# Performance work log

Hardware: AMD Instinct MI355X
Metric: run time of the kernel (lower is better)

Reference implementation:

```python
import jax, jax.numpy as jnp
import numpy as np

BLOCK_M, BLOCK_K = 16, 64
THRES = 0.8


def setup_inputs() -> dict:
    key = jax.random.key(0)
    kx, kw = jax.random.split(key)
    bsz, seq, in_f, out_f = 128, 1, 4096, 11008
    x = jax.random.normal(kx, (bsz, seq, in_f), dtype=jnp.float16)
    # kaiming_uniform_(a=sqrt(5)) on a (in,out) weight -> bound = 1/sqrt(fan_in)
    bound = 1.0 / np.sqrt(in_f)
    weight = jax.random.uniform(kw, (in_f, out_f), dtype=jnp.float16,
                                minval=-bound, maxval=bound)
    bias = jnp.zeros((out_f,), dtype=jnp.float16)
    return {"x": x, "weight": weight, "bias": bias}


def reference(x, weight, bias):
    bsz, seq, hidden = x.shape
    x2 = x.reshape(bsz * seq, hidden)          # (M, K), seq == 1 decode path
    M, K = x2.shape
    # avg_magnitude_threshold: per (BLOCK_M, BLOCK_K) block mean |x| vs thres
    blocks = x2.reshape(M // BLOCK_M, BLOCK_M, K // BLOCK_K, BLOCK_K)
    avg = jnp.mean(jnp.abs(blocks).astype(jnp.float32), axis=(1, 3))  # (M/bm, K/bk)
    mask = avg > THRES                           # block active if avg magnitude above thres
    # blocksparse_masked_gemm: skipped blocks contribute nothing -> zero them out
    xm = jnp.where(mask[:, None, :, None], blocks, jnp.float16(0)).reshape(M, K)
    y = xm @ weight                              # (M, out_features)
    return y.reshape(bsz, seq, -1) + bias
```

## Files before the change

### kernel.cpp

```cpp
#include <hip/hip_runtime.h>
#include <stdint.h>

using f32x4   = __attribute__((ext_vector_type(4))) float;
using short8  = __attribute__((ext_vector_type(8))) short;
using float4v = __attribute__((ext_vector_type(4))) float;
using float2v = __attribute__((ext_vector_type(2))) float;
using uint2v  = __attribute__((ext_vector_type(2))) unsigned int;
using uint4v  = __attribute__((ext_vector_type(4))) unsigned int;

#define NCOL 11008
#define KDIM 4096
#define LSTRIDE 264

__device__ __forceinline__ unsigned pk_bf16(float a, float b) {
  unsigned ua = __float_as_uint(a); ua += 0x7fffu + ((ua >> 16) & 1u);
  unsigned ub = __float_as_uint(b); ub += 0x7fffu + ((ub >> 16) & 1u);
  return (ua >> 16) | (ub & 0xffff0000u);
}

__global__ __launch_bounds__(256) void mask_convert_kernel(
    const float* __restrict__ x, unsigned* __restrict__ xbf) {
  const int rb = blockIdx.x;
  const int g  = blockIdx.y;
  const int t  = threadIdx.x;
  __shared__ double part[256];
  __shared__ unsigned sh_bits;

  const float* base = x + (size_t)rb * 16 * KDIM + g * 512 + t * 2;
  double s = 0.0;
#pragma unroll
  for (int r = 0; r < 16; ++r) {
    float2v a = *(const float2v*)(base + (size_t)r * KDIM);
    s += (double)fabsf(a[0]) + (double)fabsf(a[1]);
  }
  part[t] = s;
  __syncthreads();
  if (t < 8) {
    double acc = 0.0;
#pragma unroll
    for (int u = 0; u < 32; ++u) acc += part[t * 32 + u];
    bool on = (acc * (1.0 / 1024.0)) > (double)0.8f;
    unsigned long long bal = __ballot(on);
    if (t == 0) sh_bits = (unsigned)(bal & 0xffu);
  }
  __syncthreads();
  const unsigned keep = (sh_bits >> (t >> 5)) & 1u;

  unsigned* dst = xbf + (size_t)rb * 16 * (KDIM / 2) + g * 256 + t;
#pragma unroll
  for (int r = 0; r < 16; ++r) {
    float2v a = *(const float2v*)(base + (size_t)r * KDIM);
    dst[(size_t)r * (KDIM / 2)] = keep ? pk_bf16(a[0], a[1]) : 0u;
  }
}

__global__ __launch_bounds__(256) void gemm_kernel(
    const unsigned* __restrict__ xbf, const float* __restrict__ w,
    const float* __restrict__ bias, float* __restrict__ out) {

  __shared__ __align__(16) uint8_t lds[64 * LSTRIDE];

  const int tid  = threadIdx.x;
  const int lane = tid & 63;
  const int wv   = tid >> 6;
  const int c    = lane & 15;
  const int q    = lane >> 4;
  const int n0   = blockIdx.x * 128;
  const int kz   = blockIdx.y;

  f32x4 acc[8][2] = {};

  const int sk = tid >> 5;
  const int sn = (tid & 31) * 4;
  uint8_t* wS = lds + (size_t)sk * LSTRIDE + sn * 2;

  float4v wr[8];
#define ISSUE_W(KB)                                                      \
  {                                                                      \
    const float* wp = w + (size_t)(kz * 512 + (KB)*64 + sk) * NCOL + n0 + sn; \
    _Pragma("unroll")                                                    \
    for (int r = 0; r < 8; ++r)                                          \
      wr[r] = *(const float4v*)(wp + (size_t)r * 8 * NCOL);              \
  }

  const uint4v* aBase = (const uint4v*)xbf + (size_t)c * 512 + kz * 64 + q;

  ISSUE_W(0);
  for (int kb = 0; kb < 8; ++kb) {
    __syncthreads();
#pragma unroll
    for (int r = 0; r < 8; ++r) {
      uint2v v;
      v[0] = pk_bf16(wr[r][0], wr[r][1]);
      v[1] = pk_bf16(wr[r][2], wr[r][3]);
      *(uint2v*)(wS + (size_t)r * 8 * LSTRIDE) = v;
    }
    __syncthreads();
    if (kb < 7) ISSUE_W(kb + 1);

#pragma unroll
    for (int ks = 0; ks < 2; ++ks) {
      union { uint4v u; short8 v; } am[8];
#pragma unroll
      for (int mt = 0; mt < 8; ++mt)
        am[mt].u = aBase[(size_t)mt * 16 * 512 + kb * 8 + ks * 4];

      const uint8_t* wb = lds + (size_t)(ks * 32 + q * 8) * LSTRIDE + (wv * 32 + 2 * c) * 2;
      unsigned wj[8];
#pragma unroll
      for (int j = 0; j < 8; ++j)
        wj[j] = *(const unsigned*)(wb + (size_t)j * LSTRIDE);
      union { short8 v; unsigned u[4]; } be, bo;
#pragma unroll
      for (int p = 0; p < 4; ++p) {
        be.u[p] = (wj[2 * p] & 0x0000ffffu) | (wj[2 * p + 1] << 16);
        bo.u[p] = (wj[2 * p] >> 16) | (wj[2 * p + 1] & 0xffff0000u);
      }
#pragma unroll
      for (int mt = 0; mt < 8; ++mt) {
        acc[mt][0] = __builtin_amdgcn_mfma_f32_16x16x32_bf16(am[mt].v, be.v, acc[mt][0], 0, 0, 0);
        acc[mt][1] = __builtin_amdgcn_mfma_f32_16x16x32_bf16(am[mt].v, bo.v, acc[mt][1], 0, 0, 0);
      }
    }
  }
#undef ISSUE_W

  const int colE = n0 + wv * 32 + 2 * c;
  const float bE = (kz == 0) ? bias[colE] : 0.f;
  const float bO = (kz == 0) ? bias[colE + 1] : 0.f;
#pragma unroll
  for (int mt = 0; mt < 8; ++mt) {
#pragma unroll
    for (int p = 0; p < 4; ++p) {
      const int row = mt * 16 + q * 4 + p;
      float* o = out + (size_t)row * NCOL + colE;
      unsafeAtomicAdd(o,     acc[mt][0][p] + bE);
      unsafeAtomicAdd(o + 1, acc[mt][1][p] + bO);
    }
  }
}

extern "C" void kernel_launch(void* const* d_in, const int* in_sizes, int n_in,
                              void* d_out, int out_size, void* d_ws, size_t ws_size,
                              hipStream_t stream) {
  const float* x    = (const float*)d_in[0];
  const float* w    = (const float*)d_in[1];
  const float* bias = (const float*)d_in[2];
  float* out        = (float*)d_out;
  unsigned* xbf     = (unsigned*)d_ws;

  hipLaunchKernelGGL(mask_convert_kernel, dim3(8, 8), dim3(256), 0, stream, x, xbf);
  hipMemsetAsync(out, 0, (size_t)out_size * sizeof(float), stream);
  hipLaunchKernelGGL(gemm_kernel, dim3(86, 8), dim3(256), 0, stream,
                     xbf, w, bias, out);
}
```

Before: 329.9 us.

## Replace split-K atomics with per-row-block full-K tiles and direct stores

Changes the GEMM decomposition from split-K over 8 slices to one block per 16-row by 128-column tile running over the full K dimension. This removes the output memset and the atomic accumulation, replacing them with plain vectorized stores. In exchange, each weight tile is loaded and converted from fp32 to bf16 eight times, once per row block, instead of once. Each K step also does far fewer MFMAs between barriers, and the K loop is eight times longer.

```diff
diff --git a/kernel.cpp b/kernel.cpp
--- a/kernel.cpp
+++ b/kernel.cpp
@@ -65,28 +65,28 @@
   const int wv   = tid >> 6;
   const int c    = lane & 15;
   const int q    = lane >> 4;
-  const int n0   = blockIdx.x * 128;
-  const int kz   = blockIdx.y;
+  const int rb   = blockIdx.x;
+  const int n0   = blockIdx.y * 128;
 
-  f32x4 acc[8][2] = {};
+  f32x4 acc[2] = {};
 
   const int sk = tid >> 5;
   const int sn = (tid & 31) * 4;
   uint8_t* wS = lds + (size_t)sk * LSTRIDE + sn * 2;
 
+  const uint4v* aBase = (const uint4v*)xbf + (size_t)(rb * 16 + c) * (KDIM / 8) + q;
+
   float4v wr[8];
 #define ISSUE_W(KB)                                                      \
   {                                                                      \
-    const float* wp = w + (size_t)(kz * 512 + (KB)*64 + sk) * NCOL + n0 + sn; \
+    const float* wp = w + (size_t)((KB)*64 + sk) * NCOL + n0 + sn;       \
     _Pragma("unroll")                                                    \
     for (int r = 0; r < 8; ++r)                                          \
       wr[r] = *(const float4v*)(wp + (size_t)r * 8 * NCOL);              \
   }
 
-  const uint4v* aBase = (const uint4v*)xbf + (size_t)c * 512 + kz * 64 + q;
-
   ISSUE_W(0);
-  for (int kb = 0; kb < 8; ++kb) {
+  for (int kb = 0; kb < 64; ++kb) {
     __syncthreads();
 #pragma unroll
     for (int r = 0; r < 8; ++r) {
@@ -96,14 +96,12 @@
       *(uint2v*)(wS + (size_t)r * 8 * LSTRIDE) = v;
     }
     __syncthreads();
-    if (kb < 7) ISSUE_W(kb + 1);
+    if (kb < 63) ISSUE_W(kb + 1);
 
 #pragma unroll
     for (int ks = 0; ks < 2; ++ks) {
-      union { uint4v u; short8 v; } am[8];
-#pragma unroll
-      for (int mt = 0; mt < 8; ++mt)
-        am[mt].u = aBase[(size_t)mt * 16 * 512 + kb * 8 + ks * 4];
+      union { uint4v u; short8 v; } am;
+      am.u = aBase[kb * 8 + ks * 4];
 
       const uint8_t* wb = lds + (size_t)(ks * 32 + q * 8) * LSTRIDE + (wv * 32 + 2 * c) * 2;
       unsigned wj[8];
@@ -116,27 +114,22 @@
         be.u[p] = (wj[2 * p] & 0x0000ffffu) | (wj[2 * p + 1] << 16);
         bo.u[p] = (wj[2 * p] >> 16) | (wj[2 * p + 1] & 0xffff0000u);
       }
-#pragma unroll
-      for (int mt = 0; mt < 8; ++mt) {
-        acc[mt][0] = __builtin_amdgcn_mfma_f32_16x16x32_bf16(am[mt].v, be.v, acc[mt][0], 0, 0, 0);
-        acc[mt][1] = __builtin_amdgcn_mfma_f32_16x16x32_bf16(am[mt].v, bo.v, acc[mt][1], 0, 0, 0);
-      }
+      acc[0] = __builtin_amdgcn_mfma_f32_16x16x32_bf16(am.v, be.v, acc[0], 0, 0, 0);
+      acc[1] = __builtin_amdgcn_mfma_f32_16x16x32_bf16(am.v, bo.v, acc[1], 0, 0, 0);
     }
   }
 #undef ISSUE_W
 
   const int colE = n0 + wv * 32 + 2 * c;
-  const float bE = (kz == 0) ? bias[colE] : 0.f;
-  const float bO = (kz == 0) ? bias[colE + 1] : 0.f;
+  const float bE = bias[colE];
+  const float bO = bias[colE + 1];
 #pragma unroll
-  for (int mt = 0; mt < 8; ++mt) {
-#pragma unroll
-    for (int p = 0; p < 4; ++p) {
-      const int row = mt * 16 + q * 4 + p;
-      float* o = out + (size_t)row * NCOL + colE;
-      unsafeAtomicAdd(o,     acc[mt][0][p] + bE);
-      unsafeAtomicAdd(o + 1, acc[mt][1][p] + bO);
-    }
+  for (int p = 0; p < 4; ++p) {
+    const int row = rb * 16 + q * 4 + p;
+    float2v st;
+    st[0] = acc[0][p] + bE;
+    st[1] = acc[1][p] + bO;
+    *(float2v*)(out + (size_t)row * NCOL + colE) = st;
   }
 }
 
@@ -150,7 +143,6 @@
   unsigned* xbf     = (unsigned*)d_ws;
 
   hipLaunchKernelGGL(mask_convert_kernel, dim3(8, 8), dim3(256), 0, stream, x, xbf);
-  hipMemsetAsync(out, 0, (size_t)out_size * sizeof(float), stream);
-  hipLaunchKernelGGL(gemm_kernel, dim3(86, 8), dim3(256), 0, stream,
+  hipLaunchKernelGGL(gemm_kernel, dim3(8, 86), dim3(256), 0, stream,
                      xbf, w, bias, out);
 }
```

New measurement: 412.3 us. 1.25x slower.

## Replace split-K atomic GEMM with per-block intra-block K split and LDS reduction

Applied to the files above, without the earlier changes.

The grid changes from an 86x8 split-K launch (4 waves per block, atomic adds into a memset output) to 344 blocks of 2 waves. Each block owns 32 output columns, and its two waves split K into interleaved halves. Each wave stages bf16-converted weights in a private double-buffered LDS region with a 2-deep register prefetch and no block barriers. The partial sums are combined through LDS and written with plain stores plus bias, which removes the memset and the roughly 11M float atomics. The cost is far fewer resident waves and less memory-level parallelism on a bandwidth-bound weight stream.

```diff
diff --git a/kernel.cpp b/kernel.cpp
--- a/kernel.cpp
+++ b/kernel.cpp
@@ -5,12 +5,12 @@
 using short8  = __attribute__((ext_vector_type(8))) short;
 using float4v = __attribute__((ext_vector_type(4))) float;
 using float2v = __attribute__((ext_vector_type(2))) float;
-using uint2v  = __attribute__((ext_vector_type(2))) unsigned int;
 using uint4v  = __attribute__((ext_vector_type(4))) unsigned int;
 
 #define NCOL 11008
 #define KDIM 4096
-#define LSTRIDE 264
+#define WSTRIDE 72
+#define BUFSZ (32 * WSTRIDE)
 
 __device__ __forceinline__ unsigned pk_bf16(float a, float b) {
   unsigned ua = __float_as_uint(a); ua += 0x7fffu + ((ua >> 16) & 1u);
@@ -54,88 +54,108 @@
   }
 }
 
-__global__ __launch_bounds__(256) void gemm_kernel(
+__global__ __launch_bounds__(128) void gemm_kernel(
     const unsigned* __restrict__ xbf, const float* __restrict__ w,
     const float* __restrict__ bias, float* __restrict__ out) {
 
-  __shared__ __align__(16) uint8_t lds[64 * LSTRIDE];
+  __shared__ __align__(16) uint8_t lds[16384];
 
   const int tid  = threadIdx.x;
   const int lane = tid & 63;
   const int wv   = tid >> 6;
   const int c    = lane & 15;
   const int q    = lane >> 4;
-  const int n0   = blockIdx.x * 128;
-  const int kz   = blockIdx.y;
+  const int n0   = blockIdx.x * 32;
+
+  uint8_t* myLds = lds + wv * 2 * BUFSZ;
 
   f32x4 acc[8][2] = {};
 
-  const int sk = tid >> 5;
-  const int sn = (tid & 31) * 4;
-  uint8_t* wS = lds + (size_t)sk * LSTRIDE + sn * 2;
+  const int sr = lane >> 1, sh = lane & 1;
+  const float* wBase = w + (size_t)(wv * 32 + sr) * NCOL + n0 + sh * 16;
+  const int ldsOff = sr * WSTRIDE + sh * 32;
 
-  float4v wr[8];
-#define ISSUE_W(KB)                                                      \
-  {                                                                      \
-    const float* wp = w + (size_t)(kz * 512 + (KB)*64 + sk) * NCOL + n0 + sn; \
-    _Pragma("unroll")                                                    \
-    for (int r = 0; r < 8; ++r)                                          \
-      wr[r] = *(const float4v*)(wp + (size_t)r * 8 * NCOL);              \
+  float4v wr[2][4];
+#define ISSUE_W(KB)                                                     \
+  {                                                                     \
+    const float* wp = wBase + (size_t)(KB) * 64 * NCOL;                 \
+    wr[(KB) & 1][0] = *(const float4v*)(wp);                            \
+    wr[(KB) & 1][1] = *(const float4v*)(wp + 4);                        \
+    wr[(KB) & 1][2] = *(const float4v*)(wp + 8);                        \
+    wr[(KB) & 1][3] = *(const float4v*)(wp + 12);                       \
   }
 
-  const uint4v* aBase = (const uint4v*)xbf + (size_t)c * 512 + kz * 64 + q;
+  const uint4v* aBase = (const uint4v*)xbf + (size_t)c * 512 + wv * 4 + q;
 
   ISSUE_W(0);
-  for (int kb = 0; kb < 8; ++kb) {
-    __syncthreads();
+  ISSUE_W(1);
+  for (int kb = 0; kb < 64; ++kb) {
+    const int b = kb & 1;
+    uint8_t* buf = myLds + b * BUFSZ;
+
+    uint4v v0, v1;
+    v0[0] = pk_bf16(wr[b][0][0], wr[b][0][1]);
+    v0[1] = pk_bf16(wr[b][0][2], wr[b][0][3]);
+    v0[2] = pk_bf16(wr[b][1][0], wr[b][1][1]);
+    v0[3] = pk_bf16(wr[b][1][2], wr[b][1][3]);
+    v1[0] = pk_bf16(wr[b][2][0], wr[b][2][1]);
+    v1[1] = pk_bf16(wr[b][2][2], wr[b][2][3]);
+    v1[2] = pk_bf16(wr[b][3][0], wr[b][3][1]);
+    v1[3] = pk_bf16(wr[b][3][2], wr[b][3][3]);
+    *(uint4v*)(buf + ldsOff) = v0;
+    *(uint4v*)(buf + ldsOff + 16) = v1;
+
+    if (kb < 62) ISSUE_W(kb + 2);
+
+    union { uint4v u; short8 v; } am[8];
 #pragma unroll
-    for (int r = 0; r < 8; ++r) {
-      uint2v v;
-      v[0] = pk_bf16(wr[r][0], wr[r][1]);
-      v[1] = pk_bf16(wr[r][2], wr[r][3]);
-      *(uint2v*)(wS + (size_t)r * 8 * LSTRIDE) = v;
+    for (int mt = 0; mt < 8; ++mt)
+      am[mt].u = aBase[(size_t)mt * 16 * 512 + kb * 8];
+
+    const uint8_t* wb = buf + (size_t)q * 8 * WSTRIDE + c * 4;
+    unsigned wj[8];
+#pragma unroll
+    for (int j = 0; j < 8; ++j)
+      wj[j] = *(const unsigned*)(wb + (size_t)j * WSTRIDE);
+    union { short8 v; unsigned u[4]; } be, bo;
+#pragma unroll
+    for (int p = 0; p < 4; ++p) {
+      be.u[p] = (wj[2 * p] & 0x0000ffffu) | (wj[2 * p + 1] << 16);
+      bo.u[p] = (wj[2 * p] >> 16) | (wj[2 * p + 1] & 0xffff0000u);
     }
-    __syncthreads();
-    if (kb < 7) ISSUE_W(kb + 1);
-
 #pragma unroll
-    for (int ks = 0; ks < 2; ++ks) {
-      union { uint4v u; short8 v; } am[8];
-#pragma unroll
-      for (int mt = 0; mt < 8; ++mt)
-        am[mt].u = aBase[(size_t)mt * 16 * 512 + kb * 8 + ks * 4];
-
-      const uint8_t* wb = lds + (size_t)(ks * 32 + q * 8) * LSTRIDE + (wv * 32 + 2 * c) * 2;
-      unsigned wj[8];
-#pragma unroll
-      for (int j = 0; j < 8; ++j)
-        wj[j] = *(const unsigned*)(wb + (size_t)j * LSTRIDE);
-      union { short8 v; unsigned u[4]; } be, bo;
-#pragma unroll
-      for (int p = 0; p < 4; ++p) {
-        be.u[p] = (wj[2 * p] & 0x0000ffffu) | (wj[2 * p + 1] << 16);
-        bo.u[p] = (wj[2 * p] >> 16) | (wj[2 * p + 1] & 0xffff0000u);
-      }
-#pragma unroll
-      for (int mt = 0; mt < 8; ++mt) {
-        acc[mt][0] = __builtin_amdgcn_mfma_f32_16x16x32_bf16(am[mt].v, be.v, acc[mt][0], 0, 0, 0);
-        acc[mt][1] = __builtin_amdgcn_mfma_f32_16x16x32_bf16(am[mt].v, bo.v, acc[mt][1], 0, 0, 0);
-      }
+    for (int mt = 0; mt < 8; ++mt) {
+      acc[mt][0] = __builtin_amdgcn_mfma_f32_16x16x32_bf16(am[mt].v, be.v, acc[mt][0], 0, 0, 0);
+      acc[mt][1] = __builtin_amdgcn_mfma_f32_16x16x32_bf16(am[mt].v, bo.v, acc[mt][1], 0, 0, 0);
     }
   }
 #undef ISSUE_W
 
-  const int colE = n0 + wv * 32 + 2 * c;
-  const float bE = (kz == 0) ? bias[colE] : 0.f;
-  const float bO = (kz == 0) ? bias[colE + 1] : 0.f;
+  __syncthreads();
+  if (wv == 0) {
 #pragma unroll
-  for (int mt = 0; mt < 8; ++mt) {
+    for (int mt = 0; mt < 8; ++mt)
 #pragma unroll
-    for (int p = 0; p < 4; ++p) {
-      const int row = mt * 16 + q * 4 + p;
-      float* o = out + (size_t)row * NCOL + colE;
-      unsafeAtomicAdd(o,     acc[mt][0][p] + bE);
-      unsafeAtomicAdd(o + 1, acc[mt][1][p] + bO);
+      for (int eo = 0; eo < 2; ++eo)
+        *(f32x4*)(lds + ((size_t)(mt * 2 + eo) * 64 + lane) * 16) = acc[mt][eo];
+  }
+  __syncthreads();
+  if (wv == 1) {
+    const int colE = n0 + 2 * c;
+    const float bE = bias[colE];
+    const float bO = bias[colE + 1];
+#pragma unroll
+    for (int mt = 0; mt < 8; ++mt) {
+      f32x4 pe = *(const f32x4*)(lds + ((size_t)(mt * 2 + 0) * 64 + lane) * 16);
+      f32x4 po = *(const f32x4*)(lds + ((size_t)(mt * 2 + 1) * 64 + lane) * 16);
+#pragma unroll
+      for (int p = 0; p < 4; ++p) {
+        const int row = mt * 16 + q * 4 + p;
+        float2v st;
+        st[0] = acc[mt][0][p] + pe[p] + bE;
+        st[1] = acc[mt][1][p] + po[p] + bO;
+        *(float2v*)(out + (size_t)row * NCOL + colE) = st;
+      }
     }
   }
 }
@@ -150,7 +170,6 @@
   unsigned* xbf     = (unsigned*)d_ws;
 
   hipLaunchKernelGGL(mask_convert_kernel, dim3(8, 8), dim3(256), 0, stream, x, xbf);
-  hipMemsetAsync(out, 0, (size_t)out_size * sizeof(float), stream);
-  hipLaunchKernelGGL(gemm_kernel, dim3(86, 8), dim3(256), 0, stream,
+  hipLaunchKernelGGL(gemm_kernel, dim3(344), dim3(128), 0, stream,
                      xbf, w, bias, out);
 }
```

New measurement: 350.9 us. +6.4%, slower.

## Use single-wave GEMM blocks with double-buffered LDS and split-K partial reduction

Applied to the files above, without the earlier changes.

The GEMM moves from 256-thread blocks covering 128 columns with 8-way split-K to 64-thread single-wave blocks covering 32 columns with 4-way split-K. Weight loads are double-buffered in registers and LDS with a two-stage prefetch, which lets the kernel drop __syncthreads. The memset and float atomics into the output are replaced by plain stores of per-split partials into workspace, followed by a separate reduce kernel that sums them and adds bias. This removes atomic contention and the memset, at the cost of an extra kernel launch, extra workspace traffic, and more A-tile reloads across the smaller blocks.

```diff
diff --git a/kernel.cpp b/kernel.cpp
--- a/kernel.cpp
+++ b/kernel.cpp
@@ -5,12 +5,12 @@
 using short8  = __attribute__((ext_vector_type(8))) short;
 using float4v = __attribute__((ext_vector_type(4))) float;
 using float2v = __attribute__((ext_vector_type(2))) float;
-using uint2v  = __attribute__((ext_vector_type(2))) unsigned int;
 using uint4v  = __attribute__((ext_vector_type(4))) unsigned int;
 
 #define NCOL 11008
 #define KDIM 4096
-#define LSTRIDE 264
+#define WSTRIDE 72
+#define KBUF (64 * WSTRIDE)
 
 __device__ __forceinline__ unsigned pk_bf16(float a, float b) {
   unsigned ua = __float_as_uint(a); ua += 0x7fffu + ((ua >> 16) & 1u);
@@ -54,62 +54,69 @@
   }
 }
 
-__global__ __launch_bounds__(256) void gemm_kernel(
+__global__ __launch_bounds__(64) void gemm_kernel(
     const unsigned* __restrict__ xbf, const float* __restrict__ w,
-    const float* __restrict__ bias, float* __restrict__ out) {
+    float* __restrict__ pws) {
 
-  __shared__ __align__(16) uint8_t lds[64 * LSTRIDE];
+  __shared__ __align__(16) uint8_t lds[2 * KBUF];
 
-  const int tid  = threadIdx.x;
-  const int lane = tid & 63;
-  const int wv   = tid >> 6;
+  const int lane = threadIdx.x;
   const int c    = lane & 15;
   const int q    = lane >> 4;
-  const int n0   = blockIdx.x * 128;
+  const int n0   = blockIdx.x * 32;
   const int kz   = blockIdx.y;
 
   f32x4 acc[8][2] = {};
 
-  const int sk = tid >> 5;
-  const int sn = (tid & 31) * 4;
-  uint8_t* wS = lds + (size_t)sk * LSTRIDE + sn * 2;
+  const int rr = lane >> 2, q4 = lane & 3;
+  const float* wBase = w + (size_t)(kz * 1024 + rr) * NCOL + n0 + q4 * 8;
+  const int ldsWOff = rr * WSTRIDE + q4 * 16;
 
-  float4v wr[8];
-#define ISSUE_W(KB)                                                      \
-  {                                                                      \
-    const float* wp = w + (size_t)(kz * 512 + (KB)*64 + sk) * NCOL + n0 + sn; \
-    _Pragma("unroll")                                                    \
-    for (int r = 0; r < 8; ++r)                                          \
-      wr[r] = *(const float4v*)(wp + (size_t)r * 8 * NCOL);              \
+  float4v wr[2][8];
+#define ISSUE_W(KBL)                                                    \
+  {                                                                     \
+    const float* wp = wBase + (size_t)(KBL) * 64 * NCOL;                \
+    _Pragma("unroll")                                                   \
+    for (int m = 0; m < 4; ++m) {                                       \
+      wr[(KBL) & 1][m * 2 + 0] = *(const float4v*)(wp + (size_t)m * 16 * NCOL);     \
+      wr[(KBL) & 1][m * 2 + 1] = *(const float4v*)(wp + (size_t)m * 16 * NCOL + 4); \
+    }                                                                   \
   }
 
-  const uint4v* aBase = (const uint4v*)xbf + (size_t)c * 512 + kz * 64 + q;
+  const uint4v* aBase = (const uint4v*)xbf + (size_t)c * 512 + kz * 128 + q;
 
   ISSUE_W(0);
-  for (int kb = 0; kb < 8; ++kb) {
-    __syncthreads();
+  ISSUE_W(1);
+  for (int kbl = 0; kbl < 16; ++kbl) {
+    const int b = kbl & 1;
+    uint8_t* buf = lds + b * KBUF;
+
+    union { uint4v u; short8 v; } am[2][8];
 #pragma unroll
-    for (int r = 0; r < 8; ++r) {
-      uint2v v;
-      v[0] = pk_bf16(wr[r][0], wr[r][1]);
-      v[1] = pk_bf16(wr[r][2], wr[r][3]);
-      *(uint2v*)(wS + (size_t)r * 8 * LSTRIDE) = v;
+    for (int ks = 0; ks < 2; ++ks)
+#pragma unroll
+      for (int mt = 0; mt < 8; ++mt)
+        am[ks][mt].u = aBase[(size_t)mt * 16 * 512 + kbl * 8 + ks * 4];
+
+#pragma unroll
+    for (int m = 0; m < 4; ++m) {
+      uint4v v;
+      v[0] = pk_bf16(wr[b][m * 2 + 0][0], wr[b][m * 2 + 0][1]);
+      v[1] = pk_bf16(wr[b][m * 2 + 0][2], wr[b][m * 2 + 0][3]);
+      v[2] = pk_bf16(wr[b][m * 2 + 1][0], wr[b][m * 2 + 1][1]);
+      v[3] = pk_bf16(wr[b][m * 2 + 1][2], wr[b][m * 2 + 1][3]);
+      *(uint4v*)(buf + (size_t)m * 16 * WSTRIDE + ldsWOff) = v;
     }
-    __syncthreads();
-    if (kb < 7) ISSUE_W(kb + 1);
+
+    if (kbl < 14) ISSUE_W(kbl + 2);
 
 #pragma unroll
     for (int ks = 0; ks < 2; ++ks) {
-      union { uint4v u; short8 v; } am[8];
-#pragma unroll
-      for (int mt = 0; mt < 8; ++mt)
-        am[mt].u = aBase[(size_t)mt * 16 * 512 + kb * 8 + ks * 4];
-
-      const uint8_t* wb = lds + (size_t)(ks * 32 + q * 8) * LSTRIDE + (wv * 32 + 2 * c) * 2;
+      const uint8_t* wb = buf + (size_t)(ks * 32 + q * 8) * WSTRIDE + c * 4;
       unsigned wj[8];
 #pragma unroll
       for (int j = 0; j < 8; ++j)
-        wj[j] = *(const unsigned*)(wb + (size_t)j * LSTRIDE);
+        wj[j] = *(const unsigned*)(wb + (size_t)j * WSTRIDE);
       union { short8 v; unsigned u[4]; } be, bo;
 #pragma unroll
       for (int p = 0; p < 4; ++p) {
@@ -118,26 +125,44 @@
       }
 #pragma unroll
       for (int mt = 0; mt < 8; ++mt) {
-        acc[mt][0] = __builtin_amdgcn_mfma_f32_16x16x32_bf16(am[mt].v, be.v, acc[mt][0], 0, 0, 0);
-        acc[mt][1] = __builtin_amdgcn_mfma_f32_16x16x32_bf16(am[mt].v, bo.v, acc[mt][1], 0, 0, 0);
+        acc[mt][0] = __builtin_amdgcn_mfma_f32_16x16x32_bf16(am[ks][mt].v, be.v, acc[mt][0], 0, 0, 0);
+        acc[mt][1] = __builtin_amdgcn_mfma_f32_16x16x32_bf16(am[ks][mt].v, bo.v, acc[mt][1], 0, 0, 0);
       }
     }
   }
 #undef ISSUE_W
 
-  const int colE = n0 + wv * 32 + 2 * c;
-  const float bE = (kz == 0) ? bias[colE] : 0.f;
-  const float bO = (kz == 0) ? bias[colE + 1] : 0.f;
+  float* P = pws + ((size_t)blockIdx.x * 4 + kz) * (128 * 32);
 #pragma unroll
   for (int mt = 0; mt < 8; ++mt) {
 #pragma unroll
     for (int p = 0; p < 4; ++p) {
       const int row = mt * 16 + q * 4 + p;
-      float* o = out + (size_t)row * NCOL + colE;
-      unsafeAtomicAdd(o,     acc[mt][0][p] + bE);
-      unsafeAtomicAdd(o + 1, acc[mt][1][p] + bO);
+      float2v st;
+      st[0] = acc[mt][0][p];
+      st[1] = acc[mt][1][p];
+      *(float2v*)(P + (size_t)row * 32 + 2 * c) = st;
     }
   }
+}
+
+__global__ __launch_bounds__(256) void reduce_kernel(
+    const float* __restrict__ pws, const float* __restrict__ bias,
+    float* __restrict__ out) {
+  const int idx = blockIdx.x * 256 + threadIdx.x;
+  const int c2  = idx & 15;
+  const int r   = (idx >> 4) & 127;
+  const int nt  = idx >> 11;
+  const float* p = pws + (size_t)nt * 4 * (128 * 32) + (size_t)r * 32 + c2 * 2;
+  float2v s0 = *(const float2v*)(p);
+  float2v s1 = *(const float2v*)(p + 128 * 32);
+  float2v s2 = *(const float2v*)(p + 2 * 128 * 32);
+  float2v s3 = *(const float2v*)(p + 3 * 128 * 32);
+  const int col = nt * 32 + c2 * 2;
+  float2v o;
+  o[0] = s0[0] + s1[0] + s2[0] + s3[0] + bias[col];
+  o[1] = s0[1] + s1[1] + s2[1] + s3[1] + bias[col + 1];
+  *(float2v*)(out + (size_t)r * NCOL + col) = o;
 }
 
 extern "C" void kernel_launch(void* const* d_in, const int* in_sizes, int n_in,
@@ -148,9 +173,9 @@
   const float* bias = (const float*)d_in[2];
   float* out        = (float*)d_out;
   unsigned* xbf     = (unsigned*)d_ws;
+  float* pws        = (float*)((char*)d_ws + (1u << 20));
 
   hipLaunchKernelGGL(mask_convert_kernel, dim3(8, 8), dim3(256), 0, stream, x, xbf);
-  hipMemsetAsync(out, 0, (size_t)out_size * sizeof(float), stream);
-  hipLaunchKernelGGL(gemm_kernel, dim3(86, 8), dim3(256), 0, stream,
-                     xbf, w, bias, out);
+  hipLaunchKernelGGL(gemm_kernel, dim3(344, 4), dim3(64), 0, stream, xbf, w, pws);
+  hipLaunchKernelGGL(reduce_kernel, dim3(2752), dim3(256), 0, stream, pws, bias, out);
 }
```

After: 346.8 us. +5.1%, slower.
